# Kernel optimization log

Measured on AMD Instinct MI355X. Metric: run time of the kernel, lower is better.

Reference implementation:

```python
import math
import jax, jax.numpy as jnp
import numpy as np

B, P, L, R = 16, 256, 8, 128  # n_embd = L*R = 1024
H = 4 * L * R                 # MLP hidden = 4096

def new_gelu(x):
    # tanh-approx GELU as in NewGELU
    c = math.sqrt(2.0 / math.pi)
    return 0.5 * x * (1.0 + jnp.tanh(c * (x + 0.044715 * x * x * x)))

def setup_inputs() -> dict:
    key = jax.random.key(0)
    k1, k2, k3 = jax.random.split(key, 3)
    x = jax.random.normal(k1, (B, P, L, R), dtype=jnp.float32)
    W1 = jax.random.normal(k2, (L * R, H), dtype=jnp.float32) * 0.02
    b1 = jnp.zeros((H,), dtype=jnp.float32)
    W2 = jax.random.normal(k3, (H, R), dtype=jnp.float32) * 0.02
    b2 = jnp.zeros((R,), dtype=jnp.float32)
    return {"x": x, "W1": W1, "b1": b1, "W2": W2, "b2": b2}

def reference(x, W1, b1, W2, b2):
    b, p, l, r = x.shape
    flat = x.reshape(b, p, l * r)                       # [B,P,L*R]
    # Level i input = flat with first i*R entries zeroed (zeros-pad + tail slice)
    col = jnp.arange(l * r)
    mask = (col[None, :] >= (jnp.arange(l) * r)[:, None]).astype(x.dtype)  # [L, L*R]
    inp = flat[:, :, None, :] * mask                    # [B,P,L,L*R]
    h = new_gelu(jnp.einsum('bple,eh->bplh', inp, W1) + b1)  # [B,P,L,H]
    out = jnp.einsum('bplh,hr->bplr', h, W2) + b2       # [B,P,L,R]
    return out
```

## Files before the change

### kernel.cpp

```cpp
#include <hip/hip_runtime.h>
#include <hip/hip_bf16.h>


typedef _Float16 half8 __attribute__((ext_vector_type(8)));
typedef _Float16 half4 __attribute__((ext_vector_type(4)));
typedef _Float16 half2v __attribute__((ext_vector_type(2)));
typedef float    f32x4  __attribute__((ext_vector_type(4)));
typedef float    f32x16 __attribute__((ext_vector_type(16)));

#define MFMA3216(A,B,C) __builtin_amdgcn_mfma_f32_32x32x16_f16(A, B, C, 0, 0, 0)

__device__ __forceinline__ float gelu_f(float x){
  float t2 = x * fmaf(x*x, -0.10294324f, -2.30220842f);
  float e  = __builtin_amdgcn_exp2f(t2);
  return x * __builtin_amdgcn_rcpf(1.0f + e);
}

#define XROW 1028

__global__ void k_prep(const float* __restrict__ x, const float* __restrict__ w1,
                       const float* __restrict__ w2,
                       _Float16* __restrict__ xt, _Float16* __restrict__ w1t,
                       _Float16* __restrict__ w2t){
  __shared__ _Float16 Xs[32*XROW];
  int bid = blockIdx.x;
  int t   = threadIdx.x;
  if (bid < 128){
    const float4* x4 = reinterpret_cast<const float4*>(x) + (size_t)bid*8192;
    #pragma unroll
    for (int i = 0; i < 32; ++i){
      float4 v = x4[i*256 + t];
      half4 h;
      h[0]=(_Float16)v.x; h[1]=(_Float16)v.y; h[2]=(_Float16)v.z; h[3]=(_Float16)v.w;
      *reinterpret_cast<half4*>(Xs + i*XROW + t*4) = h;
    }
    __syncthreads();
    #pragma unroll
    for (int f = 0; f < 16; ++f){
      int fragidx = f*256 + t;
      int lane = fragidx & 63, kf = fragidx >> 6;
      int tok32 = lane & 31;
      int k = kf*16 + (lane >> 5)*8;
      half8 v = *reinterpret_cast<const half8*>(Xs + tok32*XROW + k);
      *reinterpret_cast<half8*>(xt + ((size_t)bid*4096 + fragidx)*8) = v;
    }
  } else if (bid < 2176){
    int tid = (bid - 128)*256 + t;
    int lane = tid & 63;
    int ht   = (tid >> 6) & 15;
    int kf   = (tid >> 10) & 63;
    int hq   = tid >> 16;
    int n = hq*512 + ht*32 + (lane & 31);
    int k = kf*16 + (lane >> 5)*8;
    half8 v;
    #pragma unroll
    for (int jj = 0; jj < 8; ++jj) v[jj] = (_Float16)w1[(size_t)(k + jj)*4096 + n];
    *reinterpret_cast<half8*>(w1t + (size_t)tid*8) = v;
  } else {
    int tid = (bid - 2176)*256 + t;
    int lane = tid & 63;
    int rt   = (tid >> 6) & 3;
    int kf   = (tid >> 8) & 31;
    int hq   = tid >> 13;
    int n = rt*32 + (lane & 31);
    int k = hq*512 + kf*16 + (lane >> 5)*8;
    half8 v;
    #pragma unroll
    for (int jj = 0; jj < 8; ++jj) v[jj] = (_Float16)w2[(size_t)(k + jj)*128 + n];
    *reinterpret_cast<half8*>(w2t + (size_t)tid*8) = v;
  }
}

__global__ void k_init_out(const float* __restrict__ b2, float* __restrict__ out){
  int i = blockIdx.x*256 + threadIdx.x;
  float4 bv = reinterpret_cast<const float4*>(b2)[i & 31];
  reinterpret_cast<float4*>(out)[i] = bv;
}

__global__ void k_reduce(const unsigned* __restrict__ part, const float* __restrict__ b2,
                         float* __restrict__ out){
  int tid = blockIdx.x*256 + threadIdx.x;
  int r   = tid & 127;
  int tc  = (tid >> 7) & 31;
  int j   = (tid >> 12) & 7;
  int tt  = tid >> 15;
  float s0 = 0.f, s1 = 0.f;
  #pragma unroll
  for (int hq = 0; hq < 8; ++hq){
    unsigned v = __builtin_nontemporal_load(part + (size_t)hq*2097152 + tid);
    half2v h = __builtin_bit_cast(half2v, v);
    s0 += (float)h[0];
    s1 += (float)h[1];
  }
  int tka = tt*64 + (tc >> 3)*16 + (tc & 7);
  float bb = b2[r];
  out[(size_t)tka*1024 + j*128 + r]       = s0 + bb;
  out[(size_t)(tka+8)*1024 + j*128 + r]   = s1 + bb;
}

__global__ __launch_bounds__(1024, 4) void k_treemlp(
    const _Float16* __restrict__ xt, const _Float16* __restrict__ w1t,
    const _Float16* __restrict__ w2t, const float* __restrict__ b1,
    unsigned* __restrict__ partial, float* __restrict__ out, int use_partial){
  int b    = blockIdx.x;
  int hq   = b & 7;
  int tt   = b >> 3;
  int t    = threadIdx.x;
  int w    = t >> 6;
  int lane = t & 63;
  int t32 = lane & 31, q2 = lane >> 5;

  __shared__ _Float16 Pbuf[2][32768];
  __shared__ _Float16 Xls[2][8192];

  f32x16 acc1[2][2];
  if (w < 8){
    #pragma unroll
    for (int hf = 0; hf < 2; ++hf){
      int base = hq*512 + (w*2 + hf)*32;
      #pragma unroll
      for (int g = 0; g < 4; ++g){
        float4 bv = *reinterpret_cast<const float4*>(b1 + base + 8*g + 4*q2);
        #pragma unroll
        for (int c = 0; c < 4; ++c){
          acc1[hf][0][g*4 + c] = ((const float*)&bv)[c];
          acc1[hf][1][g*4 + c] = ((const float*)&bv)[c];
        }
      }
    }
  }

  {
    int lane_s = t & 63, s = (t >> 6) & 7, tgl = (t >> 9) & 1;
    half8 v = *reinterpret_cast<const half8*>(
        xt + (size_t)((tt*2 + tgl)*64 + 7*8 + s)*512 + lane_s*8);
    *reinterpret_cast<half8*>(&Xls[1][(size_t)t*8]) = v;
  }
  __syncthreads();

  const _Float16* w1base = w1t + (size_t)hq*524288 + (size_t)(w*2)*512 + lane*8;
  int wc = w - 8;
  int th = (wc >> 2) & 1, rt = wc & 3;
  const _Float16* w2base = w2t + ((size_t)(hq*32)*4 + rt)*512 + lane*8;

  #pragma unroll
  for (int k = 0; k < 9; ++k){
    if (w < 8){
      if (k <= 7){
        int L = 7 - k;
        if (L >= 1){
          #pragma unroll
          for (int c = 0; c < 2; ++c){
            int idx = c*512 + (w*64 + lane);
            int lane_s = idx & 63, s = (idx >> 6) & 7, tgl = idx >> 9;
            half8 v = *reinterpret_cast<const half8*>(
                xt + (size_t)((tt*2 + tgl)*64 + (L-1)*8 + s)*512 + lane_s*8);
            *reinterpret_cast<half8*>(&Xls[(L-1) & 1][(size_t)idx*8]) = v;
          }
        }
        const _Float16* xb = Xls[L & 1];
        #pragma unroll
        for (int s = 0; s < 8; ++s){
          int kfg = L*8 + s;
          half8 a0 = *reinterpret_cast<const half8*>(w1base + (size_t)(kfg*16    )*512);
          half8 a1 = *reinterpret_cast<const half8*>(w1base + (size_t)(kfg*16 + 1)*512);
          half8 x0 = *reinterpret_cast<const half8*>(&xb[(size_t)((    s)*64 + lane)*8]);
          half8 x1 = *reinterpret_cast<const half8*>(&xb[(size_t)((8 + s)*64 + lane)*8]);
          acc1[0][0] = MFMA3216(a0, x0, acc1[0][0]);
          acc1[0][1] = MFMA3216(a0, x1, acc1[0][1]);
          acc1[1][0] = MFMA3216(a1, x0, acc1[1][0]);
          acc1[1][1] = MFMA3216(a1, x1, acc1[1][1]);
        }
        _Float16* pb = Pbuf[L & 1];
        #pragma unroll
        for (int hf = 0; hf < 2; ++hf)
          #pragma unroll
          for (int tg = 0; tg < 2; ++tg)
            #pragma unroll
            for (int g2 = 0; g2 < 4; ++g2){
              half4 hv;
              #pragma unroll
              for (int rr = 0; rr < 4; ++rr)
                hv[rr] = (_Float16)gelu_f(acc1[hf][tg][g2*4 + rr]);
              int kf = (w*2 + hf)*2 + (g2 >> 1);
              *reinterpret_cast<half4*>(
                  &pb[(size_t)((tg*32 + kf)*64 + t32 + 32*(g2 & 1))*8 + 4*q2]) = hv;
            }
      }
    } else {
      if (k >= 1){
        int Lc = 8 - k;
        const _Float16* pb = Pbuf[Lc & 1];
        f32x16 outJ;
        #pragma unroll
        for (int c = 0; c < 16; ++c) outJ[c] = 0.f;
        #pragma unroll
        for (int kf = 0; kf < 32; ++kf){
          half8 wf = *reinterpret_cast<const half8*>(w2base + (size_t)kf*2048);
          half8 pf = *reinterpret_cast<const half8*>(
              &pb[(size_t)((th*32 + kf)*64 + lane)*8]);
          outJ = MFMA3216(pf, wf, outJ);
        }
        if (use_partial){
          unsigned* pbase = partial + (size_t)hq*2097152 + (size_t)tt*32768
                          + (size_t)Lc*4096;
          #pragma unroll
          for (int i = 0; i < 8; ++i){
            int gg = i >> 2, ii = i & 3;
            int lo = gg*8 + ii;
            half2v p;
            p[0] = (_Float16)outJ[lo];
            p[1] = (_Float16)outJ[lo + 4];
            int tc = (th*2 + gg)*8 + ii + 4*q2;
            __builtin_nontemporal_store(__builtin_bit_cast(unsigned, p),
                                        pbase + (size_t)tc*128 + rt*32 + t32);
          }
        } else {
          #pragma unroll
          for (int reg = 0; reg < 16; ++reg){
            int tok = tt*64 + th*32 + (reg & 3) + 8*(reg >> 2) + 4*q2;
            atomicAdd(out + (size_t)tok*1024 + Lc*128 + rt*32 + t32, outJ[reg]);
          }
        }
      }
    }
    __syncthreads();
  }
}

extern "C" void kernel_launch(void* const* d_in, const int* in_sizes, int n_in,
                              void* d_out, int out_size, void* d_ws, size_t ws_size,
                              hipStream_t stream){
  (void)in_sizes; (void)n_in; (void)out_size;
  const float* x  = (const float*)d_in[0];
  const float* W1 = (const float*)d_in[1];
  const float* b1 = (const float*)d_in[2];
  const float* W2 = (const float*)d_in[3];
  const float* b2 = (const float*)d_in[4];
  float* out = (float*)d_out;

  _Float16* xt  = (_Float16*)d_ws;
  _Float16* w1t = xt  + 4194304;
  _Float16* w2t = w1t + 4194304;
  unsigned* partial = (unsigned*)(w2t + 524288);
  const size_t need = (size_t)(4194304 + 4194304 + 524288)*2 + (size_t)16777216*4;
  int use_partial = (ws_size >= need) ? 1 : 0;

  hipLaunchKernelGGL(k_prep, dim3(2432), dim3(256), 0, stream, x, W1, W2, xt, w1t, w2t);
  if (!use_partial)
    hipLaunchKernelGGL(k_init_out, dim3(4096), dim3(256), 0, stream, b2, out);
  hipLaunchKernelGGL(k_treemlp, dim3(512), dim3(1024), 0, stream,
                     xt, w1t, w2t, b1, partial, out, use_partial);
  if (use_partial)
    hipLaunchKernelGGL(k_reduce, dim3(8192), dim3(256), 0, stream, partial, b2, out);
}
```

Measured before the change: 216.3 us.

## Shrink MLP block to 12 waves, doubling second-GEMM work per consumer wave

The consumer (W2) waves drop from 8 to 4. Each one now computes both 32-token halves, so a single W2 fragment load feeds two MFMAs and W2 global traffic per block is halved. Block size goes from 1024 to 768 threads with launch bounds of 3 blocks per CU, and the initial X tile load moves onto the producer waves. W1 and W2 fragment loads are batched ahead of the MFMA chains to hide latency, and fp16 conversions use packed round-toward-zero converts. The cost is longer consumer work per stage, which may make the producer/consumer pipeline unbalanced, plus higher register pressure per wave.

```diff
diff --git a/kernel.cpp b/kernel.cpp
--- a/kernel.cpp
+++ b/kernel.cpp
@@ -5,6 +5,7 @@
 typedef _Float16 half8 __attribute__((ext_vector_type(8)));
 typedef _Float16 half4 __attribute__((ext_vector_type(4)));
 typedef _Float16 half2v __attribute__((ext_vector_type(2)));
+typedef __fp16   fp16x2 __attribute__((ext_vector_type(2)));
 typedef float    f32x4  __attribute__((ext_vector_type(4)));
 typedef float    f32x16 __attribute__((ext_vector_type(16)));
 
@@ -98,7 +99,7 @@
   out[(size_t)(tka+8)*1024 + j*128 + r]   = s1 + bb;
 }
 
-__global__ __launch_bounds__(1024, 4) void k_treemlp(
+__global__ __launch_bounds__(768, 3) void k_treemlp(
     const _Float16* __restrict__ xt, const _Float16* __restrict__ w1t,
     const _Float16* __restrict__ w2t, const float* __restrict__ b1,
     unsigned* __restrict__ partial, float* __restrict__ out, int use_partial){
@@ -128,19 +129,19 @@
         }
       }
     }
-  }
-
-  {
-    int lane_s = t & 63, s = (t >> 6) & 7, tgl = (t >> 9) & 1;
-    half8 v = *reinterpret_cast<const half8*>(
-        xt + (size_t)((tt*2 + tgl)*64 + 7*8 + s)*512 + lane_s*8);
-    *reinterpret_cast<half8*>(&Xls[1][(size_t)t*8]) = v;
+    #pragma unroll
+    for (int c = 0; c < 2; ++c){
+      int idx = c*512 + (w*64 + lane);
+      int lane_s = idx & 63, s = (idx >> 6) & 7, tgl = idx >> 9;
+      half8 v = *reinterpret_cast<const half8*>(
+          xt + (size_t)((tt*2 + tgl)*64 + 7*8 + s)*512 + lane_s*8);
+      *reinterpret_cast<half8*>(&Xls[1][(size_t)idx*8]) = v;
+    }
   }
   __syncthreads();
 
   const _Float16* w1base = w1t + (size_t)hq*524288 + (size_t)(w*2)*512 + lane*8;
-  int wc = w - 8;
-  int th = (wc >> 2) & 1, rt = wc & 3;
+  int rt = w - 8;
   const _Float16* w2base = w2t + ((size_t)(hq*32)*4 + rt)*512 + lane*8;
 
   #pragma unroll
@@ -160,16 +161,24 @@
         }
         const _Float16* xb = Xls[L & 1];
         #pragma unroll
-        for (int s = 0; s < 8; ++s){
-          int kfg = L*8 + s;
-          half8 a0 = *reinterpret_cast<const half8*>(w1base + (size_t)(kfg*16    )*512);
-          half8 a1 = *reinterpret_cast<const half8*>(w1base + (size_t)(kfg*16 + 1)*512);
-          half8 x0 = *reinterpret_cast<const half8*>(&xb[(size_t)((    s)*64 + lane)*8]);
-          half8 x1 = *reinterpret_cast<const half8*>(&xb[(size_t)((8 + s)*64 + lane)*8]);
-          acc1[0][0] = MFMA3216(a0, x0, acc1[0][0]);
-          acc1[0][1] = MFMA3216(a0, x1, acc1[0][1]);
-          acc1[1][0] = MFMA3216(a1, x0, acc1[1][0]);
-          acc1[1][1] = MFMA3216(a1, x1, acc1[1][1]);
+        for (int c2 = 0; c2 < 2; ++c2){
+          half8 af[8];
+          #pragma unroll
+          for (int u = 0; u < 4; ++u){
+            int kfg = L*8 + c2*4 + u;
+            af[u*2    ] = *reinterpret_cast<const half8*>(w1base + (size_t)(kfg*16    )*512);
+            af[u*2 + 1] = *reinterpret_cast<const half8*>(w1base + (size_t)(kfg*16 + 1)*512);
+          }
+          #pragma unroll
+          for (int u = 0; u < 4; ++u){
+            int s = c2*4 + u;
+            half8 x0 = *reinterpret_cast<const half8*>(&xb[(size_t)((    s)*64 + lane)*8]);
+            half8 x1 = *reinterpret_cast<const half8*>(&xb[(size_t)((8 + s)*64 + lane)*8]);
+            acc1[0][0] = MFMA3216(af[u*2    ], x0, acc1[0][0]);
+            acc1[0][1] = MFMA3216(af[u*2    ], x1, acc1[0][1]);
+            acc1[1][0] = MFMA3216(af[u*2 + 1], x0, acc1[1][0]);
+            acc1[1][1] = MFMA3216(af[u*2 + 1], x1, acc1[1][1]);
+          }
         }
         _Float16* pb = Pbuf[L & 1];
         #pragma unroll
@@ -178,10 +187,13 @@
           for (int tg = 0; tg < 2; ++tg)
             #pragma unroll
             for (int g2 = 0; g2 < 4; ++g2){
+              fp16x2 lo = __builtin_amdgcn_cvt_pkrtz(
+                  gelu_f(acc1[hf][tg][g2*4 + 0]), gelu_f(acc1[hf][tg][g2*4 + 1]));
+              fp16x2 hi = __builtin_amdgcn_cvt_pkrtz(
+                  gelu_f(acc1[hf][tg][g2*4 + 2]), gelu_f(acc1[hf][tg][g2*4 + 3]));
               half4 hv;
-              #pragma unroll
-              for (int rr = 0; rr < 4; ++rr)
-                hv[rr] = (_Float16)gelu_f(acc1[hf][tg][g2*4 + rr]);
+              hv[0]=(_Float16)lo[0]; hv[1]=(_Float16)lo[1];
+              hv[2]=(_Float16)hi[0]; hv[3]=(_Float16)hi[1];
               int kf = (w*2 + hf)*2 + (g2 >> 1);
               *reinterpret_cast<half4*>(
                   &pb[(size_t)((tg*32 + kf)*64 + t32 + 32*(g2 & 1))*8 + 4*q2]) = hv;
@@ -191,35 +203,49 @@
       if (k >= 1){
         int Lc = 8 - k;
         const _Float16* pb = Pbuf[Lc & 1];
-        f32x16 outJ;
-        #pragma unroll
-        for (int c = 0; c < 16; ++c) outJ[c] = 0.f;
-        #pragma unroll
-        for (int kf = 0; kf < 32; ++kf){
-          half8 wf = *reinterpret_cast<const half8*>(w2base + (size_t)kf*2048);
-          half8 pf = *reinterpret_cast<const half8*>(
-              &pb[(size_t)((th*32 + kf)*64 + lane)*8]);
-          outJ = MFMA3216(pf, wf, outJ);
+        f32x16 o0, o1;
+        #pragma unroll
+        for (int c = 0; c < 16; ++c){ o0[c] = 0.f; o1[c] = 0.f; }
+        #pragma unroll
+        for (int c4 = 0; c4 < 4; ++c4){
+          half8 wfb[8];
+          #pragma unroll
+          for (int u = 0; u < 8; ++u)
+            wfb[u] = *reinterpret_cast<const half8*>(w2base + (size_t)(c4*8 + u)*2048);
+          #pragma unroll
+          for (int u = 0; u < 8; ++u){
+            int kf = c4*8 + u;
+            half8 p0 = *reinterpret_cast<const half8*>(&pb[(size_t)((     kf)*64 + lane)*8]);
+            half8 p1 = *reinterpret_cast<const half8*>(&pb[(size_t)((32 + kf)*64 + lane)*8]);
+            o0 = MFMA3216(p0, wfb[u], o0);
+            o1 = MFMA3216(p1, wfb[u], o1);
+          }
         }
         if (use_partial){
           unsigned* pbase = partial + (size_t)hq*2097152 + (size_t)tt*32768
                           + (size_t)Lc*4096;
           #pragma unroll
-          for (int i = 0; i < 8; ++i){
-            int gg = i >> 2, ii = i & 3;
-            int lo = gg*8 + ii;
-            half2v p;
-            p[0] = (_Float16)outJ[lo];
-            p[1] = (_Float16)outJ[lo + 4];
-            int tc = (th*2 + gg)*8 + ii + 4*q2;
-            __builtin_nontemporal_store(__builtin_bit_cast(unsigned, p),
-                                        pbase + (size_t)tc*128 + rt*32 + t32);
+          for (int th = 0; th < 2; ++th){
+            const f32x16& oJ = th ? o1 : o0;
+            #pragma unroll
+            for (int i = 0; i < 8; ++i){
+              int gg = i >> 2, ii = i & 3;
+              int lo = gg*8 + ii;
+              fp16x2 p = __builtin_amdgcn_cvt_pkrtz(oJ[lo], oJ[lo + 4]);
+              int tc = (th*2 + gg)*8 + ii + 4*q2;
+              __builtin_nontemporal_store(__builtin_bit_cast(unsigned, p),
+                                          pbase + (size_t)tc*128 + rt*32 + t32);
+            }
           }
         } else {
           #pragma unroll
-          for (int reg = 0; reg < 16; ++reg){
-            int tok = tt*64 + th*32 + (reg & 3) + 8*(reg >> 2) + 4*q2;
-            atomicAdd(out + (size_t)tok*1024 + Lc*128 + rt*32 + t32, outJ[reg]);
+          for (int th = 0; th < 2; ++th){
+            const f32x16& oJ = th ? o1 : o0;
+            #pragma unroll
+            for (int reg = 0; reg < 16; ++reg){
+              int tok = tt*64 + th*32 + (reg & 3) + 8*(reg >> 2) + 4*q2;
+              atomicAdd(out + (size_t)tok*1024 + Lc*128 + rt*32 + t32, oJ[reg]);
+            }
           }
         }
       }
@@ -249,7 +275,7 @@
   hipLaunchKernelGGL(k_prep, dim3(2432), dim3(256), 0, stream, x, W1, W2, xt, w1t, w2t);
   if (!use_partial)
     hipLaunchKernelGGL(k_init_out, dim3(4096), dim3(256), 0, stream, b2, out);
-  hipLaunchKernelGGL(k_treemlp, dim3(512), dim3(1024), 0, stream,
+  hipLaunchKernelGGL(k_treemlp, dim3(512), dim3(768), 0, stream,
                      xt, w1t, w2t, b1, partial, out, use_partial);
   if (use_partial)
     hipLaunchKernelGGL(k_reduce, dim3(8192), dim3(256), 0, stream, partial, b2, out);
```

Measured after the change: 199.3 us. 1.09x faster.
